# Kernel optimization log

Measured on AMD Instinct MI355X. Metric: run time of the kernel, lower is better.

## Reference

```python
import jax, jax.numpy as jnp
import numpy as np

B, W, F, N = 256, 512, 512, 512


def setup_inputs() -> dict:
    key = jax.random.key(0)
    k1, k2, k3, k4, k5 = jax.random.split(key, 5)
    return {
        "x": jax.random.normal(k1, (B, W, F), dtype=jnp.float32),
        "weight_k": jax.random.normal(k2, (F, N), dtype=jnp.float32),
        "weight_q": jax.random.normal(k3, (F, N), dtype=jnp.float32),
        "weight_v": jax.random.normal(k4, (F, N), dtype=jnp.float32),
        "w": jax.random.normal(k5, (W, 1), dtype=jnp.float32),
    }


def reference(x, weight_k, weight_q, weight_v, w):
    # x: (B, W, F)
    n_outputs = weight_k.shape[-1]
    # Per-word K/V projections (original loops over words; here one batched GEMM)
    K = jnp.einsum("bwf,fn->bwn", x, weight_k)  # (B, W, N)
    V = jnp.einsum("bwf,fn->bwn", x, weight_v)  # (B, W, N)
    # Per-sample query: t = x^T @ w -> (F,), q = t @ weight_q -> (N,)
    t = jnp.einsum("bwf,w->bf", x, w[:, 0])     # (B, F)
    Q = t @ weight_q                              # (B, N)
    # Scores over words, scaled, softmax across the word axis
    scores = jnp.einsum("bn,bwn->bw", Q, K) / jnp.sqrt(jnp.float32(n_outputs))
    weights = jax.nn.softmax(scores, axis=1)      # (B, W)
    # Weighted sum of V over words
    return jnp.einsum("bw,bwn->bn", weights, V)   # (B, N)
```

## Files before the change

### kernel.cpp

```cpp
#include <hip/hip_runtime.h>
#include <math.h>

#define B 256
#define W 512
#define F 512
#define N 512
#define NWAVE 16

__global__ __launch_bounds__(1024, 4) void fused_attn_kernel(
    const float* __restrict__ x,
    const float* __restrict__ Wq,
    const float* __restrict__ Wk,
    const float* __restrict__ Wv,
    const float* __restrict__ wvec,
    float* __restrict__ out)
{
    const int b    = blockIdx.x;
    const int tid  = threadIdx.x;
    const int lane = tid & 63;
    const int wv   = tid >> 6;
    const int f5   = tid & 511;
    const int half = tid >> 9;

    __shared__ float s_w[W];
    __shared__ float s_c[NWAVE][F];
    __shared__ float s_p2[2][F];
    __shared__ float s_t[F];
    __shared__ float s_q[N];
    __shared__ float s_r[F];
    __shared__ float s_m[NWAVE];
    __shared__ float s_l[NWAVE];
    __shared__ float s_cf[F];

    const float* xb = x + (size_t)b * W * F;

    if (tid < W) s_w[tid] = wvec[tid];
    __syncthreads();

    {
        float4 t0 = make_float4(0.f, 0.f, 0.f, 0.f);
        float4 t1 = make_float4(0.f, 0.f, 0.f, 0.f);
        const float* base = xb + (size_t)(wv * 32) * F;
#pragma unroll 2
        for (int i = 0; i < 32; i += 4) {
            float4 a0[4], a1[4];
#pragma unroll
            for (int j = 0; j < 4; ++j) {
                a0[j] = *(const float4*)(base + (size_t)(i + j) * F + lane * 4);
                a1[j] = *(const float4*)(base + (size_t)(i + j) * F + 256 + lane * 4);
            }
#pragma unroll
            for (int j = 0; j < 4; ++j) {
                const float ww = s_w[wv * 32 + i + j];
                t0.x += a0[j].x * ww; t0.y += a0[j].y * ww;
                t0.z += a0[j].z * ww; t0.w += a0[j].w * ww;
                t1.x += a1[j].x * ww; t1.y += a1[j].y * ww;
                t1.z += a1[j].z * ww; t1.w += a1[j].w * ww;
            }
        }
        *(float4*)&s_c[wv][lane * 4]       = t0;
        *(float4*)&s_c[wv][256 + lane * 4] = t1;
    }
    __syncthreads();

    {
        float tp = 0.f;
#pragma unroll
        for (int j = 0; j < 8; ++j) tp += s_c[half * 8 + j][f5];
        s_p2[half][f5] = tp;
    }
    __syncthreads();
    if (tid < F) s_t[tid] = s_p2[0][tid] + s_p2[1][tid];
    __syncthreads();

    {
        const int fb = half * 256;
        float q0 = 0.f, q1 = 0.f, q2 = 0.f, q3 = 0.f;
#pragma unroll 4
        for (int f = 0; f < 256; f += 4) {
            q0 += s_t[fb + f + 0] * Wq[(size_t)(fb + f + 0) * N + f5];
            q1 += s_t[fb + f + 1] * Wq[(size_t)(fb + f + 1) * N + f5];
            q2 += s_t[fb + f + 2] * Wq[(size_t)(fb + f + 2) * N + f5];
            q3 += s_t[fb + f + 3] * Wq[(size_t)(fb + f + 3) * N + f5];
        }
        s_p2[half][f5] = (q0 + q1) + (q2 + q3);
    }
    __syncthreads();
    if (tid < N) s_q[tid] = s_p2[0][tid] + s_p2[1][tid];
    __syncthreads();

    {
        const float4* wkrow = (const float4*)(Wk + (size_t)f5 * N + half * 256);
        const float4* qv4   = (const float4*)&s_q[half * 256];
        float r0 = 0.f, r1 = 0.f, r2 = 0.f, r3 = 0.f;
#pragma unroll 8
        for (int n4 = 0; n4 < 64; ++n4) {
            const float4 kv = wkrow[n4];
            const float4 qq = qv4[n4];
            r0 += kv.x * qq.x; r1 += kv.y * qq.y;
            r2 += kv.z * qq.z; r3 += kv.w * qq.w;
        }
        s_p2[half][f5] = (r0 + r1) + (r2 + r3);
    }
    __syncthreads();
    if (tid < F) s_r[tid] = (s_p2[0][tid] + s_p2[1][tid]) * 0.04419417382415922f;
    __syncthreads();

    const float4 r0 = *(const float4*)&s_r[lane * 4];
    const float4 r1 = *(const float4*)&s_r[256 + lane * 4];

    float m = -INFINITY, l = 0.f;
    float4 c0 = make_float4(0.f, 0.f, 0.f, 0.f);
    float4 c1 = make_float4(0.f, 0.f, 0.f, 0.f);

#pragma unroll 2
    for (int t = 0; t < 4; ++t) {
        const float* row = xb + (size_t)(wv * 32 + t * 8) * F;

        float4 xa0[8], xa1[8];
#pragma unroll
        for (int j = 0; j < 8; ++j) {
            xa0[j] = *(const float4*)(row + (size_t)j * F + lane * 4);
            xa1[j] = *(const float4*)(row + (size_t)j * F + 256 + lane * 4);
        }

        float d[8];
#pragma unroll
        for (int j = 0; j < 8; ++j) {
            d[j] = xa0[j].x * r0.x + xa0[j].y * r0.y
                 + xa0[j].z * r0.z + xa0[j].w * r0.w
                 + xa1[j].x * r1.x + xa1[j].y * r1.y
                 + xa1[j].z * r1.z + xa1[j].w * r1.w;
        }

#pragma unroll
        for (int off = 32; off >= 1; off >>= 1) {
#pragma unroll
            for (int j = 0; j < 8; ++j)
                d[j] += __shfl_xor(d[j], off, 64);
        }

        const float mb = fmaxf(fmaxf(fmaxf(d[0], d[1]), fmaxf(d[2], d[3])),
                               fmaxf(fmaxf(d[4], d[5]), fmaxf(d[6], d[7])));
        const float mn = fmaxf(m, mb);
        const float sc = __expf(m - mn);

        float p[8];
        float ps = 0.f;
#pragma unroll
        for (int j = 0; j < 8; ++j) {
            p[j] = __expf(d[j] - mn);
            ps += p[j];
        }
        l = l * sc + ps;

        float ax = c0.x * sc, ay = c0.y * sc, az = c0.z * sc, aw = c0.w * sc;
#pragma unroll
        for (int j = 0; j < 8; ++j) {
            ax += p[j] * xa0[j].x; ay += p[j] * xa0[j].y;
            az += p[j] * xa0[j].z; aw += p[j] * xa0[j].w;
        }
        c0 = make_float4(ax, ay, az, aw);

        ax = c1.x * sc; ay = c1.y * sc; az = c1.z * sc; aw = c1.w * sc;
#pragma unroll
        for (int j = 0; j < 8; ++j) {
            ax += p[j] * xa1[j].x; ay += p[j] * xa1[j].y;
            az += p[j] * xa1[j].z; aw += p[j] * xa1[j].w;
        }
        c1 = make_float4(ax, ay, az, aw);

        m = mn;
    }

    *(float4*)&s_c[wv][lane * 4]       = c0;
    *(float4*)&s_c[wv][256 + lane * 4] = c1;
    if (lane == 0) { s_m[wv] = m; s_l[wv] = l; }
    __syncthreads();

    float M = -INFINITY;
#pragma unroll
    for (int j = 0; j < NWAVE; ++j) M = fmaxf(M, s_m[j]);
    float L = 0.f;
    float alpha[NWAVE];
#pragma unroll
    for (int j = 0; j < NWAVE; ++j) {
        alpha[j] = __expf(s_m[j] - M);
        L += alpha[j] * s_l[j];
    }
    const float invL = 1.f / L;

    {
        float cp = 0.f;
#pragma unroll
        for (int j = 0; j < 8; ++j) cp += alpha[half * 8 + j] * s_c[half * 8 + j][f5];
        s_p2[half][f5] = cp;
    }
    __syncthreads();
    if (tid < F) s_cf[tid] = (s_p2[0][tid] + s_p2[1][tid]) * invL;
    __syncthreads();

    {
        const int fb = half * 256;
        float o0 = 0.f, o1 = 0.f, o2 = 0.f, o3 = 0.f;
#pragma unroll 4
        for (int f = 0; f < 256; f += 4) {
            o0 += s_cf[fb + f + 0] * Wv[(size_t)(fb + f + 0) * N + f5];
            o1 += s_cf[fb + f + 1] * Wv[(size_t)(fb + f + 1) * N + f5];
            o2 += s_cf[fb + f + 2] * Wv[(size_t)(fb + f + 2) * N + f5];
            o3 += s_cf[fb + f + 3] * Wv[(size_t)(fb + f + 3) * N + f5];
        }
        s_p2[half][f5] = (o0 + o1) + (o2 + o3);
    }
    __syncthreads();
    if (tid < N) out[(size_t)b * N + tid] = s_p2[0][tid] + s_p2[1][tid];
}

extern "C" void kernel_launch(void* const* d_in, const int* in_sizes, int n_in,
                              void* d_out, int out_size, void* d_ws, size_t ws_size,
                              hipStream_t stream)
{
    const float* x    = (const float*)d_in[0];
    const float* Wk   = (const float*)d_in[1];
    const float* Wq   = (const float*)d_in[2];
    const float* Wv   = (const float*)d_in[3];
    const float* wvec = (const float*)d_in[4];
    float* out = (float*)d_out;

    fused_attn_kernel<<<B, 1024, 0, stream>>>(x, Wq, Wk, Wv, wvec, out);
}
```

Before: 448.4 us.

## Split t=x^T w into separate 1024-block kernel and double-buffer x loads

Moves the per-sample reduction t = x^T w out of the fused kernel into a separate kernel launched with four blocks per sample, writing t into a workspace buffer. The aim is more parallelism for that first pass over x, which otherwise runs on only 256 blocks. The main attention loop now processes 4 rows per step with register double-buffering of the next rows' loads, to overlap memory latency with the softmax arithmetic. The cost is an extra kernel launch, a workspace round trip, and x still being read twice from memory.

Result: slower. 523.0 us (+16.6%).

```diff
diff --git a/kernel.cpp b/kernel.cpp
--- a/kernel.cpp
+++ b/kernel.cpp
@@ -5,14 +5,51 @@
 #define W 512
 #define F 512
 #define N 512
-#define NWAVE 16
-
-__global__ __launch_bounds__(1024, 4) void fused_attn_kernel(
+
+__global__ __launch_bounds__(512, 8) void tpart_kernel(
+    const float* __restrict__ x,
+    const float* __restrict__ wvec,
+    float* __restrict__ tbuf)
+{
+    const int blk = blockIdx.x;
+    const int b   = blk >> 2;
+    const int fq  = blk & 3;
+    const int tid = threadIdx.x;
+    const int wg  = tid >> 5;
+    const int fc  = tid & 31;
+
+    __shared__ float s_w[W];
+    __shared__ float s_part[16][128];
+
+    s_w[tid] = wvec[tid];
+    __syncthreads();
+
+    const float* xb = x + (size_t)b * W * F + fq * 128 + fc * 4;
+    float4 acc = make_float4(0.f, 0.f, 0.f, 0.f);
+#pragma unroll 8
+    for (int i = 0; i < 32; ++i) {
+        const float4 xv = *(const float4*)(xb + (size_t)(wg * 32 + i) * F);
+        const float  ww = s_w[wg * 32 + i];
+        acc.x += xv.x * ww; acc.y += xv.y * ww;
+        acc.z += xv.z * ww; acc.w += xv.w * ww;
+    }
+    *(float4*)&s_part[wg][fc * 4] = acc;
+    __syncthreads();
+
+    if (tid < 128) {
+        float s = 0.f;
+#pragma unroll
+        for (int j = 0; j < 16; ++j) s += s_part[j][tid];
+        tbuf[(size_t)b * N + fq * 128 + tid] = s;
+    }
+}
+
+__global__ __launch_bounds__(1024, 4) void attn_kernel(
     const float* __restrict__ x,
     const float* __restrict__ Wq,
     const float* __restrict__ Wk,
     const float* __restrict__ Wv,
-    const float* __restrict__ wvec,
+    const float* __restrict__ tbuf,
     float* __restrict__ out)
 {
     const int b    = blockIdx.x;
@@ -22,55 +59,18 @@
     const int f5   = tid & 511;
     const int half = tid >> 9;
 
-    __shared__ float s_w[W];
-    __shared__ float s_c[NWAVE][F];
+    __shared__ float s_c[16][F];
     __shared__ float s_p2[2][F];
     __shared__ float s_t[F];
     __shared__ float s_q[N];
     __shared__ float s_r[F];
-    __shared__ float s_m[NWAVE];
-    __shared__ float s_l[NWAVE];
+    __shared__ float s_m[16];
+    __shared__ float s_l[16];
     __shared__ float s_cf[F];
 
     const float* xb = x + (size_t)b * W * F;
 
-    if (tid < W) s_w[tid] = wvec[tid];
-    __syncthreads();
-
-    {
-        float4 t0 = make_float4(0.f, 0.f, 0.f, 0.f);
-        float4 t1 = make_float4(0.f, 0.f, 0.f, 0.f);
-        const float* base = xb + (size_t)(wv * 32) * F;
-#pragma unroll 2
-        for (int i = 0; i < 32; i += 4) {
-            float4 a0[4], a1[4];
-#pragma unroll
-            for (int j = 0; j < 4; ++j) {
-                a0[j] = *(const float4*)(base + (size_t)(i + j) * F + lane * 4);
-                a1[j] = *(const float4*)(base + (size_t)(i + j) * F + 256 + lane * 4);
-            }
-#pragma unroll
-            for (int j = 0; j < 4; ++j) {
-                const float ww = s_w[wv * 32 + i + j];
-                t0.x += a0[j].x * ww; t0.y += a0[j].y * ww;
-                t0.z += a0[j].z * ww; t0.w += a0[j].w * ww;
-                t1.x += a1[j].x * ww; t1.y += a1[j].y * ww;
-                t1.z += a1[j].z * ww; t1.w += a1[j].w * ww;
-            }
-        }
-        *(float4*)&s_c[wv][lane * 4]       = t0;
-        *(float4*)&s_c[wv][256 + lane * 4] = t1;
-    }
-    __syncthreads();
-
-    {
-        float tp = 0.f;
-#pragma unroll
-        for (int j = 0; j < 8; ++j) tp += s_c[half * 8 + j][f5];
-        s_p2[half][f5] = tp;
-    }
-    __syncthreads();
-    if (tid < F) s_t[tid] = s_p2[0][tid] + s_p2[1][tid];
+    if (tid < F) s_t[tid] = tbuf[(size_t)b * N + tid];
     __syncthreads();
 
     {
@@ -113,60 +113,68 @@
     float4 c0 = make_float4(0.f, 0.f, 0.f, 0.f);
     float4 c1 = make_float4(0.f, 0.f, 0.f, 0.f);
 
-#pragma unroll 2
-    for (int t = 0; t < 4; ++t) {
-        const float* row = xb + (size_t)(wv * 32 + t * 8) * F;
-
-        float4 xa0[8], xa1[8];
-#pragma unroll
-        for (int j = 0; j < 8; ++j) {
-            xa0[j] = *(const float4*)(row + (size_t)j * F + lane * 4);
-            xa1[j] = *(const float4*)(row + (size_t)j * F + 256 + lane * 4);
-        }
-
-        float d[8];
-#pragma unroll
-        for (int j = 0; j < 8; ++j) {
-            d[j] = xa0[j].x * r0.x + xa0[j].y * r0.y
-                 + xa0[j].z * r0.z + xa0[j].w * r0.w
-                 + xa1[j].x * r1.x + xa1[j].y * r1.y
-                 + xa1[j].z * r1.z + xa1[j].w * r1.w;
+    float4 xa0[2][4], xa1[2][4];
+    {
+        const float* row = xb + (size_t)(wv * 32) * F;
+#pragma unroll
+        for (int j = 0; j < 4; ++j) {
+            xa0[0][j] = *(const float4*)(row + (size_t)j * F + lane * 4);
+            xa1[0][j] = *(const float4*)(row + (size_t)j * F + 256 + lane * 4);
+        }
+    }
+
+#pragma unroll
+    for (int t = 0; t < 8; ++t) {
+        const int cur = t & 1;
+        const int nxt = cur ^ 1;
+
+        if (t < 7) {
+            const float* rown = xb + (size_t)(wv * 32 + (t + 1) * 4) * F;
+#pragma unroll
+            for (int j = 0; j < 4; ++j) {
+                xa0[nxt][j] = *(const float4*)(rown + (size_t)j * F + lane * 4);
+                xa1[nxt][j] = *(const float4*)(rown + (size_t)j * F + 256 + lane * 4);
+            }
+        }
+
+        float d[4];
+#pragma unroll
+        for (int j = 0; j < 4; ++j) {
+            d[j] = xa0[cur][j].x * r0.x + xa0[cur][j].y * r0.y
+                 + xa0[cur][j].z * r0.z + xa0[cur][j].w * r0.w
+                 + xa1[cur][j].x * r1.x + xa1[cur][j].y * r1.y
+                 + xa1[cur][j].z * r1.z + xa1[cur][j].w * r1.w;
         }
 
 #pragma unroll
         for (int off = 32; off >= 1; off >>= 1) {
 #pragma unroll
-            for (int j = 0; j < 8; ++j)
+            for (int j = 0; j < 4; ++j)
                 d[j] += __shfl_xor(d[j], off, 64);
         }
 
-        const float mb = fmaxf(fmaxf(fmaxf(d[0], d[1]), fmaxf(d[2], d[3])),
-                               fmaxf(fmaxf(d[4], d[5]), fmaxf(d[6], d[7])));
+        const float mb = fmaxf(fmaxf(d[0], d[1]), fmaxf(d[2], d[3]));
         const float mn = fmaxf(m, mb);
         const float sc = __expf(m - mn);
 
-        float p[8];
-        float ps = 0.f;
-#pragma unroll
-        for (int j = 0; j < 8; ++j) {
-            p[j] = __expf(d[j] - mn);
-            ps += p[j];
-        }
-        l = l * sc + ps;
+        float p[4];
+#pragma unroll
+        for (int j = 0; j < 4; ++j) p[j] = __expf(d[j] - mn);
+        l = l * sc + ((p[0] + p[1]) + (p[2] + p[3]));
 
         float ax = c0.x * sc, ay = c0.y * sc, az = c0.z * sc, aw = c0.w * sc;
 #pragma unroll
-        for (int j = 0; j < 8; ++j) {
-            ax += p[j] * xa0[j].x; ay += p[j] * xa0[j].y;
-            az += p[j] * xa0[j].z; aw += p[j] * xa0[j].w;
+        for (int j = 0; j < 4; ++j) {
+            ax += p[j] * xa0[cur][j].x; ay += p[j] * xa0[cur][j].y;
+            az += p[j] * xa0[cur][j].z; aw += p[j] * xa0[cur][j].w;
         }
         c0 = make_float4(ax, ay, az, aw);
 
         ax = c1.x * sc; ay = c1.y * sc; az = c1.z * sc; aw = c1.w * sc;
 #pragma unroll
-        for (int j = 0; j < 8; ++j) {
-            ax += p[j] * xa1[j].x; ay += p[j] * xa1[j].y;
-            az += p[j] * xa1[j].z; aw += p[j] * xa1[j].w;
+        for (int j = 0; j < 4; ++j) {
+            ax += p[j] * xa1[cur][j].x; ay += p[j] * xa1[cur][j].y;
+            az += p[j] * xa1[cur][j].z; aw += p[j] * xa1[cur][j].w;
         }
         c1 = make_float4(ax, ay, az, aw);
 
@@ -180,11 +188,11 @@
 
     float M = -INFINITY;
 #pragma unroll
-    for (int j = 0; j < NWAVE; ++j) M = fmaxf(M, s_m[j]);
+    for (int j = 0; j < 16; ++j) M = fmaxf(M, s_m[j]);
     float L = 0.f;
-    float alpha[NWAVE];
-#pragma unroll
-    for (int j = 0; j < NWAVE; ++j) {
+    float alpha[16];
+#pragma unroll
+    for (int j = 0; j < 16; ++j) {
         alpha[j] = __expf(s_m[j] - M);
         L += alpha[j] * s_l[j];
     }
@@ -225,7 +233,9 @@
     const float* Wq   = (const float*)d_in[2];
     const float* Wv   = (const float*)d_in[3];
     const float* wvec = (const float*)d_in[4];
-    float* out = (float*)d_out;
-
-    fused_attn_kernel<<<B, 1024, 0, stream>>>(x, Wq, Wk, Wv, wvec, out);
+    float* out  = (float*)d_out;
+    float* tbuf = (float*)d_ws;
+
+    tpart_kernel<<<B * 4, 512, 0, stream>>>(x, wvec, tbuf);
+    attn_kernel<<<B, 1024, 0, stream>>>(x, Wq, Wk, Wv, tbuf, out);
 }
```
